# Optimization experiments

Hardware: AMD Instinct MI355X
Metric: run time of the kernel (lower is better)

The kernel has to match this reference:

```python
import jax, jax.numpy as jnp
import numpy as np

EPS = 1e-5

def setup_inputs() -> dict:
    key = jax.random.key(0)
    ks = jax.random.split(key, 5)
    B, T, D = 2, 4096, 512
    x = jax.random.normal(ks[0], (B, T, D), dtype=jnp.float32)
    w_qkv = jax.random.normal(ks[1], (D, 3 * D), dtype=jnp.float32) * (1.0 / np.sqrt(D))
    w_out = jax.random.normal(ks[2], (D, D), dtype=jnp.float32) * (1.0 / np.sqrt(D))
    b_out = jnp.zeros((D,), dtype=jnp.float32)
    gamma = jnp.ones((D,), dtype=jnp.float32)
    beta = jnp.zeros((D,), dtype=jnp.float32)
    return {"x": x, "w_qkv": w_qkv, "w_out": w_out, "b_out": b_out,
            "gamma": gamma, "beta": beta}

def reference(x, w_qkv, w_out, b_out, gamma, beta):
    B, T, D = x.shape
    H = 8
    hd = D // H
    scale = 1.0 / jnp.sqrt(jnp.asarray(hd, x.dtype))
    residual = x
    # pre-norm LayerNorm
    mu = jnp.mean(x, axis=-1, keepdims=True)
    var = jnp.mean((x - mu) ** 2, axis=-1, keepdims=True)
    xn = (x - mu) / jnp.sqrt(var + EPS) * gamma + beta
    # qkv projection (no bias)
    qkv = (xn @ w_qkv).reshape(B, T, 3, H, hd)
    q, k, v = qkv[:, :, 0], qkv[:, :, 1], qkv[:, :, 2]  # (B,T,H,hd)
    # (B,H,T,T) scores with causal mask
    attn = jnp.einsum('bthd,bshd->bhts', q, k) * scale
    causal = jnp.triu(jnp.ones((T, T), dtype=bool), k=1)
    attn = jnp.where(causal[None, None], -jnp.inf, attn)
    attn = jax.nn.softmax(attn, axis=-1)
    out = jnp.einsum('bhts,bshd->bthd', attn, v).reshape(B, T, D)
    out = out @ w_out + b_out
    return out + residual
```

## Files before the change

kernel.cpp:

```cpp
#include <hip/hip_runtime.h>

typedef __attribute__((ext_vector_type(8))) short bh8;
typedef __attribute__((ext_vector_type(4))) float f32x4;
typedef unsigned short u16;

#define MFMA16 __builtin_amdgcn_mfma_f32_16x16x32_bf16

#if __has_builtin(__builtin_amdgcn_exp2f)
#define EXP2(x) __builtin_amdgcn_exp2f(x)
#else
#define EXP2(x) exp2f(x)
#endif

#define CEXP 0.18033688011112042f

__device__ __forceinline__ u16 f2bf(float f) {
  union { float f; unsigned u; } v; v.f = f;
  unsigned r = v.u + 0x7fffu + ((v.u >> 16) & 1u);
  return (u16)(r >> 16);
}

__device__ __forceinline__ unsigned cvtpk(float lo, float hi) {
  unsigned r;
  asm("v_cvt_pk_bf16_f32 %0, %1, %2" : "=v"(r) : "v"(lo), "v"(hi));
  return r;
}

__device__ __forceinline__ void gload16(void* lds, const void* g) {
  __builtin_amdgcn_global_load_lds(
      (const __attribute__((address_space(1))) unsigned int*)g,
      (__attribute__((address_space(3))) unsigned int*)lds, 16, 0, 0);
}

__global__ __launch_bounds__(256) void k_ln(const float* __restrict__ x,
                                            const float* __restrict__ gamma,
                                            const float* __restrict__ beta,
                                            u16* __restrict__ xn) {
  int row  = blockIdx.x * 4 + (threadIdx.x >> 6);
  int lane = threadIdx.x & 63;
  const float4* xr = (const float4*)(x + row * 512);
  float4 a = xr[lane * 2], b = xr[lane * 2 + 1];
  float s  = a.x + a.y + a.z + a.w + b.x + b.y + b.z + b.w;
  float ss = a.x*a.x + a.y*a.y + a.z*a.z + a.w*a.w
           + b.x*b.x + b.y*b.y + b.z*b.z + b.w*b.w;
#pragma unroll
  for (int m = 1; m < 64; m <<= 1) { s += __shfl_xor(s, m, 64); ss += __shfl_xor(ss, m, 64); }
  float mu  = s * (1.0f / 512.0f);
  float var = ss * (1.0f / 512.0f) - mu * mu;
  float rstd = rsqrtf(var + 1e-5f);
  const float4* g4 = (const float4*)gamma;
  const float4* b4 = (const float4*)beta;
  float4 g0 = g4[lane * 2], g1 = g4[lane * 2 + 1];
  float4 e0 = b4[lane * 2], e1 = b4[lane * 2 + 1];
  bh8 ov;
  ov[0] = (short)f2bf((a.x - mu) * rstd * g0.x + e0.x);
  ov[1] = (short)f2bf((a.y - mu) * rstd * g0.y + e0.y);
  ov[2] = (short)f2bf((a.z - mu) * rstd * g0.z + e0.z);
  ov[3] = (short)f2bf((a.w - mu) * rstd * g0.w + e0.w);
  ov[4] = (short)f2bf((b.x - mu) * rstd * g1.x + e1.x);
  ov[5] = (short)f2bf((b.y - mu) * rstd * g1.y + e1.y);
  ov[6] = (short)f2bf((b.z - mu) * rstd * g1.z + e1.z);
  ov[7] = (short)f2bf((b.w - mu) * rstd * g1.w + e1.w);
  *(bh8*)(xn + row * 512 + lane * 8) = ov;
}

__global__ __launch_bounds__(256) void k_transpose_cast(const float* __restrict__ in,
                                                        u16* __restrict__ out,
                                                        int R, int C) {
  __shared__ float tile[32][33];
  int c0 = blockIdx.x * 32, r0 = blockIdx.y * 32;
  int tx = threadIdx.x & 31, ty = threadIdx.x >> 5;
#pragma unroll
  for (int i = 0; i < 32; i += 8)
    tile[ty + i][tx] = in[(r0 + ty + i) * C + (c0 + tx)];
  __syncthreads();
#pragma unroll
  for (int i = 0; i < 32; i += 8)
    out[(c0 + ty + i) * R + (r0 + tx)] = f2bf(tile[tx][ty + i]);
}

__global__ __launch_bounds__(256) void k_repack_vt(const u16* __restrict__ V,
                                                   u16* __restrict__ Vt) {
  __shared__ u16 tile[64 * 64];
  int bh = blockIdx.y;
  int t0 = blockIdx.x * 64;
  int tid = threadIdx.x;
  const u16* src = V + (bh * 4096 + t0) * 64;
#pragma unroll
  for (int j = 0; j < 2; ++j)
    *(bh8*)&tile[(j * 256 + tid) * 8] = *(const bh8*)(src + (j * 256 + tid) * 8);
  __syncthreads();
  int d = tid >> 2, ts = (tid & 3) * 16;
  bh8 o0, o1;
#pragma unroll
  for (int e = 0; e < 8; ++e) {
    o0[e] = (short)tile[(ts + e) * 64 + d];
    o1[e] = (short)tile[(ts + 8 + e) * 64 + d];
  }
  u16* dst = Vt + (bh * 64 + d) * 4096 + t0 + ts;
  *(bh8*)dst = o0;
  *(bh8*)(dst + 8) = o1;
}

template <int EPI>
__global__ __launch_bounds__(256) void k_gemm(const u16* __restrict__ A,
                                              const u16* __restrict__ Bt,
                                              int N,
                                              u16* __restrict__ q, u16* __restrict__ kk, u16* __restrict__ v,
                                              const float* __restrict__ bias,
                                              const float* __restrict__ resid,
                                              float* __restrict__ outp) {
  constexpr int K = 512, BM = 128, BK = 64;
  __shared__ u16 Al[BM * BK];
  __shared__ u16 Bl[BM * BK];
  int nBN = N / 128;
  int bid = (blockIdx.x & 7) * (gridDim.x >> 3) + (blockIdx.x >> 3);
  int m0 = (bid / nBN) * BM;
  int n0 = (bid % nBN) * 128;
  int tid = threadIdx.x, lane = tid & 63, w = tid >> 6;
  int l16 = lane & 15, lh = lane >> 4;
  int wm = (w >> 1) * 64, wn = (w & 1) * 64;
  const u16* Ab = A + m0 * K;
  const u16* Bb = Bt + n0 * K;
  f32x4 acc[4][4];
#pragma unroll
  for (int i = 0; i < 4; ++i)
#pragma unroll
    for (int j = 0; j < 4; ++j) acc[i][j] = (f32x4){0.f, 0.f, 0.f, 0.f};
  int srow = tid >> 3, schunk = tid & 7;
  for (int k0 = 0; k0 < K; k0 += BK) {
    __syncthreads();
#pragma unroll
    for (int j = 0; j < 4; ++j) {
      int r = j * 32 + srow;
      int sc = ((schunk ^ (r & 7)) << 3);
      gload16((char*)Al + j * 4096 + tid * 16, Ab + r * K + k0 + sc);
      gload16((char*)Bl + j * 4096 + tid * 16, Bb + r * K + k0 + sc);
    }
    __syncthreads();
#pragma unroll
    for (int c = 0; c < 2; ++c) {
      bh8 af[4], bf[4];
#pragma unroll
      for (int i = 0; i < 4; ++i) {
        int ra = wm + i * 16 + l16;
        af[i] = *(const bh8*)&Al[ra * 64 + ((c * 32 + lh * 8) ^ ((ra & 7) << 3))];
        int rb = wn + i * 16 + l16;
        bf[i] = *(const bh8*)&Bl[rb * 64 + ((c * 32 + lh * 8) ^ ((rb & 7) << 3))];
      }
#pragma unroll
      for (int mi = 0; mi < 4; ++mi)
#pragma unroll
        for (int ni = 0; ni < 4; ++ni)
          acc[mi][ni] = MFMA16(af[mi], bf[ni], acc[mi][ni], 0, 0, 0);
    }
  }
  if (EPI == 0) {
#pragma unroll
    for (int mi = 0; mi < 4; ++mi)
#pragma unroll
      for (int ni = 0; ni < 4; ++ni) {
        int col = n0 + wn + ni * 16 + l16;
        int s = col >> 9, h = (col >> 6) & 7, d = col & 63;
        u16* base = (s == 0 ? q : (s == 1 ? kk : v));
#pragma unroll
        for (int j = 0; j < 4; ++j) {
          int row = m0 + wm + mi * 16 + lh * 4 + j;
          int b = row >> 12, t = row & 4095;
          base[(((b << 3) + h) * 4096 + t) * 64 + d] = f2bf(acc[mi][ni][j]);
        }
      }
  } else {
#pragma unroll
    for (int mi = 0; mi < 4; ++mi)
#pragma unroll
      for (int ni = 0; ni < 4; ++ni) {
        int col = n0 + wn + ni * 16 + l16;
        float bo = bias[col];
#pragma unroll
        for (int j = 0; j < 4; ++j) {
          int row = m0 + wm + mi * 16 + lh * 4 + j;
          outp[row * 512 + col] = acc[mi][ni][j] + bo + resid[row * 512 + col];
        }
      }
  }
}

__global__ __launch_bounds__(256) void k_attn(const u16* __restrict__ Q,
                                              const u16* __restrict__ Kg,
                                              const u16* __restrict__ Vt,
                                              u16* __restrict__ O) {
  __shared__ u16 Kl[2 * 64 * 64];
  __shared__ u16 Vl[2 * 64 * 64];
  __shared__ u16 Pl[4 * 1024];
  int bh = blockIdx.x & 15;
  int qi = 63 - (blockIdx.x >> 4);
  int tid = threadIdx.x, lane = tid & 63, w = tid >> 6;
  int l16 = lane & 15, lh = lane >> 4;
  const u16* Qb = Q + bh * 4096 * 64;
  const u16* Kb = Kg + bh * 4096 * 64;
  const u16* Vb = Vt + bh * 64 * 4096;
  int q0 = qi * 64;
  int myq = q0 + w * 16 + l16;
  bh8 qf0 = *(const bh8*)(Qb + myq * 64 + lh * 8);
  bh8 qf1 = *(const bh8*)(Qb + myq * 64 + 32 + lh * 8);
  float m_ = -3e38f, l_ = 0.f;
  f32x4 acc[4];
#pragma unroll
  for (int dn = 0; dn < 4; ++dn) acc[dn] = (f32x4){0.f, 0.f, 0.f, 0.f};
  int srow = tid >> 3, schunk = tid & 7;
  u16* pw = Pl + w * 1024 + l16 * 64;
  int pswz = (l16 & 7) << 3;

  for (int kt = 0; kt <= qi; kt += 2) {
    __syncthreads();
#pragma unroll
    for (int t = 0; t < 2; ++t) {
      int kk = (kt + t) * 64;
#pragma unroll
      for (int j = 0; j < 2; ++j) {
        int r = j * 32 + srow;
        int sc = ((schunk ^ (r & 7)) << 3);
        gload16((char*)Kl + t * 8192 + j * 4096 + tid * 16, Kb + (kk + r) * 64 + sc);
        gload16((char*)Vl + t * 8192 + j * 4096 + tid * 16, Vb + r * 4096 + kk + sc);
      }
    }
    __syncthreads();
    int k0 = kt * 64;
    f32x4 s[8];
    __builtin_amdgcn_s_setprio(1);
#pragma unroll
    for (int g = 0; g < 8; ++g) {
      const u16* Kc = Kl + (g >> 2) * 4096;
      int r = (g & 3) * 16 + l16;
      bh8 kf0 = *(const bh8*)&Kc[r * 64 + ((lh * 8) ^ ((r & 7) << 3))];
      bh8 kf1 = *(const bh8*)&Kc[r * 64 + ((32 + lh * 8) ^ ((r & 7) << 3))];
      f32x4 z = (f32x4){0.f, 0.f, 0.f, 0.f};
      z = MFMA16(kf0, qf0, z, 0, 0, 0);
      z = MFMA16(kf1, qf1, z, 0, 0, 0);
      s[g] = z;
    }
    __builtin_amdgcn_s_setprio(0);
    if (kt + 2 > qi) {
#pragma unroll
      for (int g = 0; g < 8; ++g)
#pragma unroll
        for (int j = 0; j < 4; ++j) {
          int tk = k0 + g * 16 + lh * 4 + j;
          if (tk > myq) s[g][j] = -3e38f;
        }
    }
    float mg[8];
#pragma unroll
    for (int g = 0; g < 8; ++g)
      mg[g] = fmaxf(fmaxf(s[g][0], s[g][1]), fmaxf(s[g][2], s[g][3]));
    float mx = fmaxf(fmaxf(fmaxf(mg[0], mg[1]), fmaxf(mg[2], mg[3])),
                     fmaxf(fmaxf(mg[4], mg[5]), fmaxf(mg[6], mg[7])));
    mx = fmaxf(mx, __shfl_xor(mx, 16, 64));
    mx = fmaxf(mx, __shfl_xor(mx, 32, 64));
    float nm = fmaxf(m_, mx);
    float nmC = nm * CEXP;
    float rs = 0.f;
#pragma unroll
    for (int g = 0; g < 8; ++g) {
      float p0 = EXP2(fmaf(s[g][0], CEXP, -nmC));
      float p1 = EXP2(fmaf(s[g][1], CEXP, -nmC));
      float p2 = EXP2(fmaf(s[g][2], CEXP, -nmC));
      float p3 = EXP2(fmaf(s[g][3], CEXP, -nmC));
      rs += (p0 + p1) + (p2 + p3);
      s[g][0] = p0; s[g][1] = p1; s[g][2] = p2; s[g][3] = p3;
    }
    rs += __shfl_xor(rs, 16, 64);
    rs += __shfl_xor(rs, 32, 64);
    if (__any(mx > m_)) {
      float fac = EXP2(fmaf(m_, CEXP, -nmC));
      l_ = l_ * fac + rs;
      float f0 = __shfl(fac, lh * 4 + 0, 64);
      float f1 = __shfl(fac, lh * 4 + 1, 64);
      float f2 = __shfl(fac, lh * 4 + 2, 64);
      float f3 = __shfl(fac, lh * 4 + 3, 64);
#pragma unroll
      for (int dn = 0; dn < 4; ++dn) {
        acc[dn][0] *= f0; acc[dn][1] *= f1;
        acc[dn][2] *= f2; acc[dn][3] *= f3;
      }
    } else {
      l_ += rs;
    }
    m_ = nm;
#pragma unroll
    for (int h = 0; h < 2; ++h) {
#pragma unroll
      for (int f = 0; f < 4; ++f) {
        int g = h * 4 + f;
        uint2 pk;
        pk.x = cvtpk(s[g][0], s[g][1]);
        pk.y = cvtpk(s[g][2], s[g][3]);
        *(uint2*)&pw[(f * 16 + lh * 4) ^ pswz] = pk;
      }
      bh8 pa0 = *(const bh8*)&pw[(lh * 8) ^ pswz];
      bh8 pa1 = *(const bh8*)&pw[(32 + lh * 8) ^ pswz];
      const u16* Vc = Vl + h * 4096;
      __builtin_amdgcn_s_setprio(1);
#pragma unroll
      for (int dn = 0; dn < 4; ++dn) {
        int r = dn * 16 + l16;
        const u16* vr = Vc + r * 64;
        bh8 vb0 = *(const bh8*)&vr[(lh * 8) ^ ((r & 7) << 3)];
        bh8 vb1 = *(const bh8*)&vr[(32 + lh * 8) ^ ((r & 7) << 3)];
        acc[dn] = MFMA16(pa0, vb0, acc[dn], 0, 0, 0);
        acc[dn] = MFMA16(pa1, vb1, acc[dn], 0, 0, 0);
      }
      __builtin_amdgcn_s_setprio(0);
    }
  }
  float inv = 1.0f / l_;
  float i0 = __shfl(inv, lh * 4 + 0, 64);
  float i1 = __shfl(inv, lh * 4 + 1, 64);
  float i2 = __shfl(inv, lh * 4 + 2, 64);
  float i3 = __shfl(inv, lh * 4 + 3, 64);
  int b = bh >> 3, h = bh & 7;
#pragma unroll
  for (int j = 0; j < 4; ++j) {
    float iv = (j == 0 ? i0 : j == 1 ? i1 : j == 2 ? i2 : i3);
    int t = q0 + w * 16 + lh * 4 + j;
#pragma unroll
    for (int dn = 0; dn < 4; ++dn)
      O[(b * 4096 + t) * 512 + h * 64 + dn * 16 + l16] = f2bf(acc[dn][j] * iv);
  }
}

extern "C" void kernel_launch(void* const* d_in, const int* in_sizes, int n_in,
                              void* d_out, int out_size, void* d_ws, size_t ws_size,
                              hipStream_t stream) {
  const float* x     = (const float*)d_in[0];
  const float* w_qkv = (const float*)d_in[1];
  const float* w_out = (const float*)d_in[2];
  const float* b_out = (const float*)d_in[3];
  const float* gamma = (const float*)d_in[4];
  const float* beta  = (const float*)d_in[5];
  float* out = (float*)d_out;
  char* ws = (char*)d_ws;
  u16* xn    = (u16*)(ws);
  u16* wqkvT = (u16*)(ws + 8388608);
  u16* woutT = (u16*)(ws + 9961472);
  u16* q     = (u16*)(ws + 10485760);
  u16* k     = (u16*)(ws + 18874368);
  u16* v     = (u16*)(ws + 27262976);
  u16* vt       = xn;
  u16* attn_out = v;

  k_ln<<<2048, 256, 0, stream>>>(x, gamma, beta, xn);
  k_transpose_cast<<<dim3(48, 16), 256, 0, stream>>>(w_qkv, wqkvT, 512, 1536);
  k_transpose_cast<<<dim3(16, 16), 256, 0, stream>>>(w_out, woutT, 512, 512);
  k_gemm<0><<<64 * 12, 256, 0, stream>>>(xn, wqkvT, 1536, q, k, v, nullptr, nullptr, nullptr);
  k_repack_vt<<<dim3(64, 16), 256, 0, stream>>>(v, vt);
  k_attn<<<1024, 256, 0, stream>>>(q, k, vt, attn_out);
  k_gemm<1><<<64 * 4, 256, 0, stream>>>(attn_out, woutT, 512, nullptr, nullptr, nullptr, b_out, x, out);
}
```

Measured before the change: 131.3 us.

## Fuse V transpose into QKV GEMM epilogue and read V directly from global

The QKV projection epilogue now writes V straight into the transposed (d-major) layout with packed bf16 stores, removing the separate repack kernel and its extra pass over V. The attention kernel no longer stages V tiles into shared memory and instead loads V fragments directly from global memory inside the PV MFMA loop. This cuts a launch, LDS footprint, and copy traffic, but exposes global-load latency in the inner loop and relies on cache hits for repeated V reads across query blocks.

```diff
diff --git a/kernel.cpp b/kernel.cpp
--- a/kernel.cpp
+++ b/kernel.cpp
@@ -79,34 +79,11 @@
     out[(c0 + ty + i) * R + (r0 + tx)] = f2bf(tile[tx][ty + i]);
 }
 
-__global__ __launch_bounds__(256) void k_repack_vt(const u16* __restrict__ V,
-                                                   u16* __restrict__ Vt) {
-  __shared__ u16 tile[64 * 64];
-  int bh = blockIdx.y;
-  int t0 = blockIdx.x * 64;
-  int tid = threadIdx.x;
-  const u16* src = V + (bh * 4096 + t0) * 64;
-#pragma unroll
-  for (int j = 0; j < 2; ++j)
-    *(bh8*)&tile[(j * 256 + tid) * 8] = *(const bh8*)(src + (j * 256 + tid) * 8);
-  __syncthreads();
-  int d = tid >> 2, ts = (tid & 3) * 16;
-  bh8 o0, o1;
-#pragma unroll
-  for (int e = 0; e < 8; ++e) {
-    o0[e] = (short)tile[(ts + e) * 64 + d];
-    o1[e] = (short)tile[(ts + 8 + e) * 64 + d];
-  }
-  u16* dst = Vt + (bh * 64 + d) * 4096 + t0 + ts;
-  *(bh8*)dst = o0;
-  *(bh8*)(dst + 8) = o1;
-}
-
 template <int EPI>
 __global__ __launch_bounds__(256) void k_gemm(const u16* __restrict__ A,
                                               const u16* __restrict__ Bt,
                                               int N,
-                                              u16* __restrict__ q, u16* __restrict__ kk, u16* __restrict__ v,
+                                              u16* __restrict__ q, u16* __restrict__ kk, u16* __restrict__ vt,
                                               const float* __restrict__ bias,
                                               const float* __restrict__ resid,
                                               float* __restrict__ outp) {
@@ -162,12 +139,18 @@
       for (int ni = 0; ni < 4; ++ni) {
         int col = n0 + wn + ni * 16 + l16;
         int s = col >> 9, h = (col >> 6) & 7, d = col & 63;
-        u16* base = (s == 0 ? q : (s == 1 ? kk : v));
-#pragma unroll
-        for (int j = 0; j < 4; ++j) {
-          int row = m0 + wm + mi * 16 + lh * 4 + j;
-          int b = row >> 12, t = row & 4095;
-          base[(((b << 3) + h) * 4096 + t) * 64 + d] = f2bf(acc[mi][ni][j]);
+        int row0 = m0 + wm + mi * 16 + lh * 4;
+        int b = row0 >> 12, t0 = row0 & 4095;
+        if (s == 2) {
+          uint2 pk;
+          pk.x = cvtpk(acc[mi][ni][0], acc[mi][ni][1]);
+          pk.y = cvtpk(acc[mi][ni][2], acc[mi][ni][3]);
+          *(uint2*)&vt[((size_t)((b << 3) + h) * 64 + d) * 4096 + t0] = pk;
+        } else {
+          u16* base = (s == 0 ? q : kk);
+#pragma unroll
+          for (int j = 0; j < 4; ++j)
+            base[(((size_t)(b << 3) + h) * 4096 + t0 + j) * 64 + d] = f2bf(acc[mi][ni][j]);
         }
       }
   } else {
@@ -191,7 +174,6 @@
                                               const u16* __restrict__ Vt,
                                               u16* __restrict__ O) {
   __shared__ u16 Kl[2 * 64 * 64];
-  __shared__ u16 Vl[2 * 64 * 64];
   __shared__ u16 Pl[4 * 1024];
   int bh = blockIdx.x & 15;
   int qi = 63 - (blockIdx.x >> 4);
@@ -199,7 +181,7 @@
   int l16 = lane & 15, lh = lane >> 4;
   const u16* Qb = Q + bh * 4096 * 64;
   const u16* Kb = Kg + bh * 4096 * 64;
-  const u16* Vb = Vt + bh * 64 * 4096;
+  const u16* Vb = Vt + (size_t)bh * 64 * 4096;
   int q0 = qi * 64;
   int myq = q0 + w * 16 + l16;
   bh8 qf0 = *(const bh8*)(Qb + myq * 64 + lh * 8);
@@ -222,7 +204,6 @@
         int r = j * 32 + srow;
         int sc = ((schunk ^ (r & 7)) << 3);
         gload16((char*)Kl + t * 8192 + j * 4096 + tid * 16, Kb + (kk + r) * 64 + sc);
-        gload16((char*)Vl + t * 8192 + j * 4096 + tid * 16, Vb + r * 4096 + kk + sc);
       }
     }
     __syncthreads();
@@ -300,14 +281,14 @@
       }
       bh8 pa0 = *(const bh8*)&pw[(lh * 8) ^ pswz];
       bh8 pa1 = *(const bh8*)&pw[(32 + lh * 8) ^ pswz];
-      const u16* Vc = Vl + h * 4096;
+      const u16* Vc = Vb + (kt + h) * 64;
       __builtin_amdgcn_s_setprio(1);
 #pragma unroll
       for (int dn = 0; dn < 4; ++dn) {
         int r = dn * 16 + l16;
-        const u16* vr = Vc + r * 64;
-        bh8 vb0 = *(const bh8*)&vr[(lh * 8) ^ ((r & 7) << 3)];
-        bh8 vb1 = *(const bh8*)&vr[(32 + lh * 8) ^ ((r & 7) << 3)];
+        const u16* vr = Vc + (size_t)r * 4096;
+        bh8 vb0 = *(const bh8*)(vr + lh * 8);
+        bh8 vb1 = *(const bh8*)(vr + 32 + lh * 8);
         acc[dn] = MFMA16(pa0, vb0, acc[dn], 0, 0, 0);
         acc[dn] = MFMA16(pa1, vb1, acc[dn], 0, 0, 0);
       }
@@ -346,15 +327,13 @@
   u16* woutT = (u16*)(ws + 9961472);
   u16* q     = (u16*)(ws + 10485760);
   u16* k     = (u16*)(ws + 18874368);
-  u16* v     = (u16*)(ws + 27262976);
-  u16* vt       = xn;
-  u16* attn_out = v;
+  u16* vt    = (u16*)(ws + 27262976);
+  u16* attn_out = xn;
 
   k_ln<<<2048, 256, 0, stream>>>(x, gamma, beta, xn);
   k_transpose_cast<<<dim3(48, 16), 256, 0, stream>>>(w_qkv, wqkvT, 512, 1536);
   k_transpose_cast<<<dim3(16, 16), 256, 0, stream>>>(w_out, woutT, 512, 512);
-  k_gemm<0><<<64 * 12, 256, 0, stream>>>(xn, wqkvT, 1536, q, k, v, nullptr, nullptr, nullptr);
-  k_repack_vt<<<dim3(64, 16), 256, 0, stream>>>(v, vt);
+  k_gemm<0><<<64 * 12, 256, 0, stream>>>(xn, wqkvT, 1536, q, k, vt, nullptr, nullptr, nullptr);
   k_attn<<<1024, 256, 0, stream>>>(q, k, vt, attn_out);
   k_gemm<1><<<64 * 4, 256, 0, stream>>>(attn_out, woutT, 512, nullptr, nullptr, nullptr, b_out, x, out);
 }
```

New measurement: 219.1 us. 1.67x slower.
